# Optimization experiments

Measured on AMD Instinct MI355X. Metric: run time of the kernel, lower is better.

## Reference

```python
import jax, jax.numpy as jnp
import numpy as np
from jax import lax

RADIUS = (5, 5, 5)
EPS = 1e-5


def _box_sum(x, radius=RADIUS):
    # Separable all-ones box filter == F.conv3d(x, ones((1,1,)+radius), padding='same')
    # x: [N, 1, D, H, W]
    dn = lax.conv_dimension_numbers(x.shape, (1, 1) + radius, ('NCDHW', 'OIDHW', 'NCDHW'))
    for axis, k in zip((2, 3, 4), radius):
        kshape = [1, 1, 1, 1, 1]
        kshape[axis] = k
        kern = jnp.ones(kshape, dtype=x.dtype)
        dn_ax = lax.conv_dimension_numbers(x.shape, tuple(kshape), ('NCDHW', 'OIDHW', 'NCDHW'))
        x = lax.conv_general_dilated(x, kern, window_strides=(1, 1, 1), padding='SAME',
                                     dimension_numbers=dn_ax)
    return x


def _image_gradient(img):
    # torch.gradient over spatial dims (central diff interior, one-sided edges)
    g = jnp.gradient(img, axis=(2, 3, 4))
    return jnp.concatenate(g, axis=1)  # [N, 3, D, H, W]


def setup_inputs() -> dict:
    key = jax.random.key(0)
    k1, k2, k3, k4 = jax.random.split(key, 4)
    shape = (1, 1, 192, 192, 192)
    moving_image = jax.random.normal(k1, shape, dtype=jnp.float32)
    fixed_image = jax.random.normal(k2, shape, dtype=jnp.float32)
    moving_mask = jax.random.randint(k3, shape, 0, 2).astype(jnp.bool_)
    fixed_mask = jax.random.randint(k4, shape, 0, 2).astype(jnp.bool_)
    original_image_spacing = jnp.ones((3,), dtype=jnp.int32)
    return {
        'moving_image': moving_image,
        'fixed_image': fixed_image,
        'moving_mask': moving_mask,
        'fixed_mask': fixed_mask,
        'original_image_spacing': original_image_spacing,
    }


def reference(moving_image, fixed_image, moving_mask, fixed_mask, original_image_spacing):
    npix = float(np.prod(RADIUS))  # 125

    # dual method: union mask applied to both gradients, total grad halved
    union = jnp.logical_or(moving_mask, fixed_mask).astype(moving_image.dtype)
    grad_moving = _image_gradient(moving_image) * union
    grad_fixed = _image_gradient(fixed_image) * union
    total_grad = (grad_moving + grad_fixed) * 0.5

    sum_m = _box_sum(moving_image)
    sum_f = _box_sum(fixed_image)
    sum_mm = _box_sum(moving_image * moving_image)
    sum_ff = _box_sum(fixed_image * fixed_image)
    sum_mf = _box_sum(moving_image * fixed_image)

    moving_mean = sum_m / npix
    fixed_mean = sum_f / npix

    var_m = sum_mm - 2 * moving_mean * sum_m + npix * moving_mean * moving_mean
    var_f = sum_ff - 2 * fixed_mean * sum_f + npix * fixed_mean * fixed_mean
    var_mf = var_m * var_f
    cross = sum_mf - fixed_mean * sum_m - moving_mean * sum_f + npix * moving_mean * fixed_mean

    moving_mean_centered = moving_image - moving_mean
    fixed_mean_centered = fixed_image - fixed_mean

    mask = (var_mf > EPS) & (var_f > EPS) & (fixed_mean_centered != 0.0) & (moving_mean_centered != 0.0)
    var_mf_safe = jnp.where(mask, var_mf, 1.0)
    var_f_safe = jnp.where(mask, var_f, 1.0)
    factor = jnp.where(
        mask,
        2.0 * cross / var_mf_safe * (moving_mean_centered - cross * fixed_mean_centered / var_f_safe),
        0.0,
    )

    return -1.0 * factor * total_grad
```

## Files before the change

### kernel.cpp

```cpp
#include <hip/hip_runtime.h>


#define DD 192
#define HH 192
#define WW 192
#define NVOX (DD * HH * WW)
#define TS 16
#define RT (TS + 4)
#define ZSEG 24

__global__ __launch_bounds__(256)
void ncc_forces_kernel(const float* __restrict__ mimg,
                       const float* __restrict__ fimg,
                       const int*   __restrict__ mmask,
                       const int*   __restrict__ fmask,
                       float* __restrict__ out)
{
    __shared__ float rawm[4][RT][RT];
    __shared__ float rawf[4][RT][RT];
    __shared__ float xs[5][RT][TS];

    const int tx = threadIdx.x;
    const int ty = threadIdx.y;
    const int tid = ty * TS + tx;
    const int x0 = blockIdx.x * TS;
    const int y0 = blockIdx.y * TS;
    const int z0 = blockIdx.z * ZSEG;
    const int z1 = z0 + ZSEG;

    float ring[5][5];
#pragma unroll
    for (int s = 0; s < 5; ++s)
#pragma unroll
        for (int f = 0; f < 5; ++f) ring[s][f] = 0.f;

    for (int zc = z0 - 2; zc <= z1 + 1; ++zc) {
        const int s4 = (zc + 4) & 3;
        const bool zin = (zc >= 0) && (zc < DD);

        for (int i = tid; i < RT * RT; i += 256) {
            const int iy = i / RT;
            const int ix = i - iy * RT;
            const int gx = x0 - 2 + ix;
            const int gy = y0 - 2 + iy;
            float vm = 0.f, vf = 0.f;
            if (zin && gx >= 0 && gx < WW && gy >= 0 && gy < HH) {
                const int gidx = (zc * HH + gy) * WW + gx;
                vm = mimg[gidx];
                vf = fimg[gidx];
            }
            rawm[s4][iy][ix] = vm;
            rawf[s4][iy][ix] = vf;
        }
        __syncthreads();

        for (int i = tid; i < RT * TS; i += 256) {
            const int y  = i >> 4;
            const int xo = i & 15;
            float sm = 0.f, sf = 0.f, smm = 0.f, sff = 0.f, smf = 0.f;
#pragma unroll
            for (int dx = 0; dx < 5; ++dx) {
                const float a = rawm[s4][y][xo + dx];
                const float b = rawf[s4][y][xo + dx];
                sm += a; sf += b; smm += a * a; sff += b * b; smf += a * b;
            }
            xs[0][y][xo] = sm;
            xs[1][y][xo] = sf;
            xs[2][y][xo] = smm;
            xs[3][y][xo] = sff;
            xs[4][y][xo] = smf;
        }
        __syncthreads();

        float s2d[5];
#pragma unroll
        for (int f = 0; f < 5; ++f) {
            float s = 0.f;
#pragma unroll
            for (int dy = 0; dy < 5; ++dy) s += xs[f][ty + dy][tx];
            s2d[f] = s;
        }
#pragma unroll
        for (int s = 0; s < 4; ++s)
#pragma unroll
            for (int f = 0; f < 5; ++f) ring[s][f] = ring[s + 1][f];
#pragma unroll
        for (int f = 0; f < 5; ++f) ring[4][f] = s2d[f];

        const int z = zc - 2;
        if (z >= z0 && z < z1) {
            float sum_m = 0.f, sum_f = 0.f, sum_mm = 0.f, sum_ff = 0.f, sum_mf = 0.f;
#pragma unroll
            for (int s = 0; s < 5; ++s) {
                sum_m  += ring[s][0];
                sum_f  += ring[s][1];
                sum_mm += ring[s][2];
                sum_ff += ring[s][3];
                sum_mf += ring[s][4];
            }
            const int gx = x0 + tx, gy = y0 + ty;
            const int sz  = (z + 4) & 3;
            const int szm = (z + 3) & 3;
            const int szp = (z + 5) & 3;
            const int cy = ty + 2, cx = tx + 2;
            const float mc = rawm[sz][cy][cx];
            const float fc = rawf[sz][cy][cx];

            float gxm, gxf, gym, gyf, gzm, gzf;
            if (gx == 0)          { gxm = rawm[sz][cy][cx + 1] - mc;  gxf = rawf[sz][cy][cx + 1] - fc; }
            else if (gx == WW-1)  { gxm = mc - rawm[sz][cy][cx - 1];  gxf = fc - rawf[sz][cy][cx - 1]; }
            else {
                gxm = 0.5f * (rawm[sz][cy][cx + 1] - rawm[sz][cy][cx - 1]);
                gxf = 0.5f * (rawf[sz][cy][cx + 1] - rawf[sz][cy][cx - 1]);
            }
            if (gy == 0)          { gym = rawm[sz][cy + 1][cx] - mc;  gyf = rawf[sz][cy + 1][cx] - fc; }
            else if (gy == HH-1)  { gym = mc - rawm[sz][cy - 1][cx];  gyf = fc - rawf[sz][cy - 1][cx]; }
            else {
                gym = 0.5f * (rawm[sz][cy + 1][cx] - rawm[sz][cy - 1][cx]);
                gyf = 0.5f * (rawf[sz][cy + 1][cx] - rawf[sz][cy - 1][cx]);
            }
            if (z == 0)           { gzm = rawm[szp][cy][cx] - mc;     gzf = rawf[szp][cy][cx] - fc; }
            else if (z == DD-1)   { gzm = mc - rawm[szm][cy][cx];     gzf = fc - rawf[szm][cy][cx]; }
            else {
                gzm = 0.5f * (rawm[szp][cy][cx] - rawm[szm][cy][cx]);
                gzf = 0.5f * (rawf[szp][cy][cx] - rawf[szm][cy][cx]);
            }

            const int vidx = (z * HH + gy) * WW + gx;
            const float u = ((mmask[vidx] != 0) || (fmask[vidx] != 0)) ? 1.0f : 0.0f;

            const float npix = 125.0f;
            const float mean_m = sum_m / npix;
            const float mean_f = sum_f / npix;
            const float var_m = sum_mm - 2.0f * mean_m * sum_m + npix * mean_m * mean_m;
            const float var_f = sum_ff - 2.0f * mean_f * sum_f + npix * mean_f * mean_f;
            const float var_mf = var_m * var_f;
            const float cross = sum_mf - mean_f * sum_m - mean_m * sum_f + npix * mean_m * mean_f;
            const float mmc = mc - mean_m;
            const float fmc = fc - mean_f;
            const bool ok = (var_mf > 1e-5f) && (var_f > 1e-5f) && (fmc != 0.0f) && (mmc != 0.0f);
            float factor = 0.0f;
            if (ok) factor = 2.0f * cross / var_mf * (mmc - cross * fmc / var_f);

            const float nf = -factor * 0.5f * u;
            out[vidx]            = nf * (gzm + gzf);
            out[NVOX + vidx]     = nf * (gym + gyf);
            out[2 * NVOX + vidx] = nf * (gxm + gxf);
        }
        __syncthreads();
    }
}

extern "C" void kernel_launch(void* const* d_in, const int* in_sizes, int n_in,
                              void* d_out, int out_size, void* d_ws, size_t ws_size,
                              hipStream_t stream)
{
    const float* mimg  = (const float*)d_in[0];
    const float* fimg  = (const float*)d_in[1];
    const int*   mmask = (const int*)d_in[2];
    const int*   fmask = (const int*)d_in[3];
    float* out = (float*)d_out;

    dim3 grid(WW / TS, HH / TS, DD / ZSEG);
    dim3 block(TS, TS, 1);
    hipLaunchKernelGGL(ncc_forces_kernel, grid, block, 0, stream,
                       mimg, fimg, mmask, fmask, out);
}
```

Baseline: 258.7 us.

## Replace shared-memory tiled box filter with register sliding-window and DPP x-sums

Rewrites the kernel so each wavefront covers a 60-wide x strip and 4 output rows, keeping running z-sums in registers (adding the incoming slice and subtracting the outgoing one) instead of re-summing a 5-slice ring. The x-direction box sums and x-gradients use DPP wave shifts rather than shared memory, which removes all LDS traffic and __syncthreads. Block indices are remapped for locality and mask loads are made nontemporal. In exchange, z-row halo values are loaded twice (incoming and outgoing slices), halo lanes do redundant work, and register pressure is high under a 3-block occupancy bound.

```diff
diff --git a/kernel.cpp b/kernel.cpp
--- a/kernel.cpp
+++ b/kernel.cpp
@@ -5,149 +5,159 @@
 #define HH 192
 #define WW 192
 #define NVOX (DD * HH * WW)
-#define TS 16
-#define RT (TS + 4)
-#define ZSEG 24
+#define ZS 12
+#define NZS 16
+#define YG 48
+#define ROWS 8
+#define RING 6
 
-__global__ __launch_bounds__(256)
+__device__ __forceinline__ float wsr1(float v) {
+    return __int_as_float(__builtin_amdgcn_update_dpp(0, __float_as_int(v), 0x138, 0xF, 0xF, true));
+}
+__device__ __forceinline__ float wsl1(float v) {
+    return __int_as_float(__builtin_amdgcn_update_dpp(0, __float_as_int(v), 0x130, 0xF, 0xF, true));
+}
+
+__global__ __launch_bounds__(256, 3)
 void ncc_forces_kernel(const float* __restrict__ mimg,
                        const float* __restrict__ fimg,
                        const int*   __restrict__ mmask,
                        const int*   __restrict__ fmask,
                        float* __restrict__ out)
 {
-    __shared__ float rawm[4][RT][RT];
-    __shared__ float rawf[4][RT][RT];
-    __shared__ float xs[5][RT][TS];
+    const int b  = blockIdx.x;
+    const int L  = (b & 7) * 96 + (b >> 3);
+    const int zs = L / YG;
+    const int yg = L - zs * YG;
+    const int w    = threadIdx.x >> 6;
+    const int lane = threadIdx.x & 63;
 
-    const int tx = threadIdx.x;
-    const int ty = threadIdx.y;
-    const int tid = ty * TS + tx;
-    const int x0 = blockIdx.x * TS;
-    const int y0 = blockIdx.y * TS;
-    const int z0 = blockIdx.z * ZSEG;
-    const int z1 = z0 + ZSEG;
+    const int x0 = w * 60;
+    const int gx = x0 + lane - 2;
+    const int y0 = yg * 4;
+    const int zstart = zs * ZS;
+    const bool gxok = (gx >= 0) && (gx < WW);
+    const bool emitlane = (lane >= 2) && (lane < 62) && (gx < WW);
 
-    float ring[5][5];
+    float sums[ROWS][5];
 #pragma unroll
-    for (int s = 0; s < 5; ++s)
+    for (int r = 0; r < ROWS; ++r)
 #pragma unroll
-        for (int f = 0; f < 5; ++f) ring[s][f] = 0.f;
+        for (int f = 0; f < 5; ++f) sums[r][f] = 0.f;
+    float rm[RING][4], rf[RING][4];
+#pragma unroll
+    for (int rr = 0; rr < RING; ++rr)
+#pragma unroll
+        for (int k = 0; k < 4; ++k) { rm[rr][k] = 0.f; rf[rr][k] = 0.f; }
 
-    for (int zc = z0 - 2; zc <= z1 + 1; ++zc) {
-        const int s4 = (zc + 4) & 3;
-        const bool zin = (zc >= 0) && (zc < DD);
+    for (int n = 0; n <= ZS + 4; ++n) {
+        const int zl = zstart - 2 + n;
+        const int zo = zl - 5;
+        const int z_out = zstart + n - 5;
+        const bool doload = (n < ZS + 4);
+        const bool dosub  = doload && (n >= 5);
+        const bool emitv  = (n >= 5);
 
-        for (int i = tid; i < RT * RT; i += 256) {
-            const int iy = i / RT;
-            const int ix = i - iy * RT;
-            const int gx = x0 - 2 + ix;
-            const int gy = y0 - 2 + iy;
-            float vm = 0.f, vf = 0.f;
-            if (zin && gx >= 0 && gx < WW && gy >= 0 && gy < HH) {
-                const int gidx = (zc * HH + gy) * WW + gx;
-                vm = mimg[gidx];
-                vf = fimg[gidx];
+        float fm[ROWS], fff[ROWS], om[ROWS], off[ROWS];
+#pragma unroll
+        for (int r = 0; r < ROWS; ++r) {
+            const int gy = y0 - 2 + r;
+            const bool yok = (gy >= 0) && (gy < HH) && gxok;
+            const bool fok = doload && yok && (zl >= 0) && (zl < DD);
+            const bool ook = dosub  && yok && (zo >= 0) && (zo < DD);
+            const size_t fi = ((size_t)zl * HH + gy) * WW + gx;
+            const size_t oi = ((size_t)zo * HH + gy) * WW + gx;
+            fm[r]  = fok ? mimg[fi] : 0.f;
+            fff[r] = fok ? fimg[fi] : 0.f;
+            om[r]  = ook ? mimg[oi] : 0.f;
+            off[r] = ook ? fimg[oi] : 0.f;
+        }
+        int um[4], uf[4];
+#pragma unroll
+        for (int j = 0; j < 4; ++j) { um[j] = 0; uf[j] = 0; }
+        if (emitv && emitlane) {
+#pragma unroll
+            for (int j = 0; j < 4; ++j) {
+                const int vidx = (z_out * HH + (y0 + j)) * WW + gx;
+                um[j] = __builtin_nontemporal_load(mmask + vidx);
+                uf[j] = __builtin_nontemporal_load(fmask + vidx);
             }
-            rawm[s4][iy][ix] = vm;
-            rawf[s4][iy][ix] = vf;
         }
-        __syncthreads();
 
-        for (int i = tid; i < RT * TS; i += 256) {
-            const int y  = i >> 4;
-            const int xo = i & 15;
-            float sm = 0.f, sf = 0.f, smm = 0.f, sff = 0.f, smf = 0.f;
+        if (emitv) {
 #pragma unroll
-            for (int dx = 0; dx < 5; ++dx) {
-                const float a = rawm[s4][y][xo + dx];
-                const float b = rawf[s4][y][xo + dx];
-                sm += a; sf += b; smm += a * a; sff += b * b; smf += a * b;
+            for (int j = 0; j < 4; ++j) {
+                const int gy = y0 + j;
+                float box[5];
+#pragma unroll
+                for (int f = 0; f < 5; ++f) {
+                    const float s = sums[j][f] + sums[j + 1][f] + sums[j + 2][f]
+                                  + sums[j + 3][f] + sums[j + 4][f];
+                    const float t1 = wsr1(s), t2 = wsr1(t1);
+                    const float u1 = wsl1(s), u2 = wsl1(u1);
+                    box[f] = s + t1 + t2 + u1 + u2;
+                }
+                const float mc = rm[j + 1][2], fc = rf[j + 1][2];
+
+                const float mxm = wsr1(mc), mxp = wsl1(mc);
+                const float fxm = wsr1(fc), fxp = wsl1(fc);
+                float gxm_, gxf_, gym_, gyf_, gzm_, gzf_;
+                if (gx == 0)           { gxm_ = mxp - mc;  gxf_ = fxp - fc; }
+                else if (gx == WW - 1) { gxm_ = mc - mxm;  gxf_ = fc - fxm; }
+                else                   { gxm_ = 0.5f * (mxp - mxm); gxf_ = 0.5f * (fxp - fxm); }
+
+                if (gy == 0)           { gym_ = rm[j + 2][2] - mc;  gyf_ = rf[j + 2][2] - fc; }
+                else if (gy == HH - 1) { gym_ = mc - rm[j][2];      gyf_ = fc - rf[j][2]; }
+                else { gym_ = 0.5f * (rm[j + 2][2] - rm[j][2]); gyf_ = 0.5f * (rf[j + 2][2] - rf[j][2]); }
+
+                if (z_out == 0)           { gzm_ = rm[j + 1][1] - mc;  gzf_ = rf[j + 1][1] - fc; }
+                else if (z_out == DD - 1) { gzm_ = mc - rm[j + 1][3];  gzf_ = fc - rf[j + 1][3]; }
+                else { gzm_ = 0.5f * (rm[j + 1][1] - rm[j + 1][3]); gzf_ = 0.5f * (rf[j + 1][1] - rf[j + 1][3]); }
+
+                const float u = ((um[j] | uf[j]) != 0) ? 1.0f : 0.0f;
+
+                const float npix = 125.0f;
+                const float inv_npix = 1.0f / 125.0f;
+                const float mean_m = box[0] * inv_npix;
+                const float mean_f = box[1] * inv_npix;
+                const float var_m = box[2] - 2.0f * mean_m * box[0] + npix * mean_m * mean_m;
+                const float var_f = box[3] - 2.0f * mean_f * box[1] + npix * mean_f * mean_f;
+                const float var_mf = var_m * var_f;
+                const float cross = box[4] - mean_f * box[0] - mean_m * box[1]
+                                  + npix * mean_m * mean_f;
+                const float mmc = mc - mean_m;
+                const float fmc = fc - mean_f;
+                const bool ok = (var_mf > 1e-5f) && (var_f > 1e-5f) && (fmc != 0.0f) && (mmc != 0.0f);
+                float factor = 0.0f;
+                if (ok) factor = 2.0f * cross / var_mf * (mmc - cross * fmc / var_f);
+
+                if (emitlane) {
+                    const int vidx = (z_out * HH + gy) * WW + gx;
+                    const float nf = -factor * 0.5f * u;
+                    out[vidx]            = nf * (gzm_ + gzf_);
+                    out[NVOX + vidx]     = nf * (gym_ + gyf_);
+                    out[2 * NVOX + vidx] = nf * (gxm_ + gxf_);
+                }
             }
-            xs[0][y][xo] = sm;
-            xs[1][y][xo] = sf;
-            xs[2][y][xo] = smm;
-            xs[3][y][xo] = sff;
-            xs[4][y][xo] = smf;
         }
-        __syncthreads();
 
-        float s2d[5];
+        if (doload) {
 #pragma unroll
-        for (int f = 0; f < 5; ++f) {
-            float s = 0.f;
+            for (int r = 0; r < ROWS; ++r) {
+                sums[r][0] += fm[r] - om[r];
+                sums[r][1] += fff[r] - off[r];
+                sums[r][2] += fm[r] * fm[r]  - om[r] * om[r];
+                sums[r][3] += fff[r] * fff[r] - off[r] * off[r];
+                sums[r][4] += fm[r] * fff[r] - om[r] * off[r];
+            }
 #pragma unroll
-            for (int dy = 0; dy < 5; ++dy) s += xs[f][ty + dy][tx];
-            s2d[f] = s;
+            for (int rr = 0; rr < RING; ++rr) {
+                rm[rr][3] = rm[rr][2]; rm[rr][2] = rm[rr][1]; rm[rr][1] = rm[rr][0];
+                rm[rr][0] = fm[rr + 1];
+                rf[rr][3] = rf[rr][2]; rf[rr][2] = rf[rr][1]; rf[rr][1] = rf[rr][0];
+                rf[rr][0] = fff[rr + 1];
+            }
         }
-#pragma unroll
-        for (int s = 0; s < 4; ++s)
-#pragma unroll
-            for (int f = 0; f < 5; ++f) ring[s][f] = ring[s + 1][f];
-#pragma unroll
-        for (int f = 0; f < 5; ++f) ring[4][f] = s2d[f];
-
-        const int z = zc - 2;
-        if (z >= z0 && z < z1) {
-            float sum_m = 0.f, sum_f = 0.f, sum_mm = 0.f, sum_ff = 0.f, sum_mf = 0.f;
-#pragma unroll
-            for (int s = 0; s < 5; ++s) {
-                sum_m  += ring[s][0];
-                sum_f  += ring[s][1];
-                sum_mm += ring[s][2];
-                sum_ff += ring[s][3];
-                sum_mf += ring[s][4];
-            }
-            const int gx = x0 + tx, gy = y0 + ty;
-            const int sz  = (z + 4) & 3;
-            const int szm = (z + 3) & 3;
-            const int szp = (z + 5) & 3;
-            const int cy = ty + 2, cx = tx + 2;
-            const float mc = rawm[sz][cy][cx];
-            const float fc = rawf[sz][cy][cx];
-
-            float gxm, gxf, gym, gyf, gzm, gzf;
-            if (gx == 0)          { gxm = rawm[sz][cy][cx + 1] - mc;  gxf = rawf[sz][cy][cx + 1] - fc; }
-            else if (gx == WW-1)  { gxm = mc - rawm[sz][cy][cx - 1];  gxf = fc - rawf[sz][cy][cx - 1]; }
-            else {
-                gxm = 0.5f * (rawm[sz][cy][cx + 1] - rawm[sz][cy][cx - 1]);
-                gxf = 0.5f * (rawf[sz][cy][cx + 1] - rawf[sz][cy][cx - 1]);
-            }
-            if (gy == 0)          { gym = rawm[sz][cy + 1][cx] - mc;  gyf = rawf[sz][cy + 1][cx] - fc; }
-            else if (gy == HH-1)  { gym = mc - rawm[sz][cy - 1][cx];  gyf = fc - rawf[sz][cy - 1][cx]; }
-            else {
-                gym = 0.5f * (rawm[sz][cy + 1][cx] - rawm[sz][cy - 1][cx]);
-                gyf = 0.5f * (rawf[sz][cy + 1][cx] - rawf[sz][cy - 1][cx]);
-            }
-            if (z == 0)           { gzm = rawm[szp][cy][cx] - mc;     gzf = rawf[szp][cy][cx] - fc; }
-            else if (z == DD-1)   { gzm = mc - rawm[szm][cy][cx];     gzf = fc - rawf[szm][cy][cx]; }
-            else {
-                gzm = 0.5f * (rawm[szp][cy][cx] - rawm[szm][cy][cx]);
-                gzf = 0.5f * (rawf[szp][cy][cx] - rawf[szm][cy][cx]);
-            }
-
-            const int vidx = (z * HH + gy) * WW + gx;
-            const float u = ((mmask[vidx] != 0) || (fmask[vidx] != 0)) ? 1.0f : 0.0f;
-
-            const float npix = 125.0f;
-            const float mean_m = sum_m / npix;
-            const float mean_f = sum_f / npix;
-            const float var_m = sum_mm - 2.0f * mean_m * sum_m + npix * mean_m * mean_m;
-            const float var_f = sum_ff - 2.0f * mean_f * sum_f + npix * mean_f * mean_f;
-            const float var_mf = var_m * var_f;
-            const float cross = sum_mf - mean_f * sum_m - mean_m * sum_f + npix * mean_m * mean_f;
-            const float mmc = mc - mean_m;
-            const float fmc = fc - mean_f;
-            const bool ok = (var_mf > 1e-5f) && (var_f > 1e-5f) && (fmc != 0.0f) && (mmc != 0.0f);
-            float factor = 0.0f;
-            if (ok) factor = 2.0f * cross / var_mf * (mmc - cross * fmc / var_f);
-
-            const float nf = -factor * 0.5f * u;
-            out[vidx]            = nf * (gzm + gzf);
-            out[NVOX + vidx]     = nf * (gym + gyf);
-            out[2 * NVOX + vidx] = nf * (gxm + gxf);
-        }
-        __syncthreads();
     }
 }
 
@@ -161,8 +171,8 @@
     const int*   fmask = (const int*)d_in[3];
     float* out = (float*)d_out;
 
-    dim3 grid(WW / TS, HH / TS, DD / ZSEG);
-    dim3 block(TS, TS, 1);
+    dim3 grid(8 * 96, 1, 1);
+    dim3 block(256, 1, 1);
     hipLaunchKernelGGL(ncc_forces_kernel, grid, block, 0, stream,
                        mimg, fimg, mmask, fmask, out);
 }
```

New measurement: 261.0 us. About the same (+0.9%).
